# Optimization experiments

Measured on AMD Instinct MI355X. Metric: run time of the kernel, lower is better.

Reference implementation:

```python
import jax, jax.numpy as jnp
import numpy as np

B, L, H, E, MODES = 32, 2048, 8, 64, 64
SCALE = 1.0 / (512 * 512)  # 1/(in_channels*out_channels)


def setup_inputs() -> dict:
    key = jax.random.key(0)
    kq, kk, kv, kwr, kwi = jax.random.split(key, 5)
    # frequency mode selection: shuffled range(L//2), first MODES, sorted (get_frequency_modes)
    rng = np.random.default_rng(0)
    index = np.sort(rng.permutation(L // 2)[:MODES]).astype(np.int32)
    return {
        "q": jax.random.normal(kq, (B, L, H, E), dtype=jnp.float32),
        "k": jax.random.normal(kk, (B, L, H, E), dtype=jnp.float32),
        "v": jax.random.normal(kv, (B, L, H, E), dtype=jnp.float32),
        "w_real": SCALE * jax.random.uniform(kwr, (H, E, E, MODES), dtype=jnp.float32),
        "w_imag": SCALE * jax.random.uniform(kwi, (H, E, E, MODES), dtype=jnp.float32),
        "index": jnp.asarray(index),
    }


def reference(q, k, v, w_real, w_imag, index):
    # q: [B, L, H, E]; k, v unused by FourierBlock
    Bq, Lq, Hq, Eq = q.shape
    x = jnp.transpose(q, (0, 2, 3, 1))            # [B, H, E, L]
    x_ft = jnp.fft.rfft(x, axis=-1)               # [B, H, E, L//2+1] complex
    xs = jnp.take(x_ft, index, axis=-1)           # gather selected modes: [B, H, E, M]
    W = w_real + 1j * w_imag                      # [H, E, E, M] complex
    # vectorized per-mode complex einsum ('bhi,hio->bho' over all modes m)
    out = jnp.einsum('bhim,hiom->bhom', xs, W)    # [B, H, E, M]
    n_freq = Lq // 2 + 1
    # original writes mode wi into slot wi (0..M-1), rest stay zero
    out_ft = jnp.concatenate(
        [out, jnp.zeros((Bq, Hq, Eq, n_freq - out.shape[-1]), dtype=out.dtype)], axis=-1)
    return jnp.fft.irfft(out_ft, n=Lq, axis=-1)   # [B, H, E, L] real
```

## Files before the change

### kernel.cpp

```cpp
#include <hip/hip_runtime.h>
#include <math.h>

#define NB 32
#define NL 2048
#define NH 8
#define NE 64
#define NM 64
#define MRI 128
#define BK 128
#define NCH 16

typedef __attribute__((ext_vector_type(8))) __bf16 bf16x8;
typedef __attribute__((ext_vector_type(2))) __bf16 bf16x2;
typedef __attribute__((ext_vector_type(8))) unsigned short us8;
typedef __attribute__((ext_vector_type(4))) unsigned short us4;
typedef __attribute__((ext_vector_type(4))) float f32x4;
typedef __attribute__((ext_vector_type(16))) float f32x16;

__device__ __forceinline__ unsigned short f2bf(float x) {
  unsigned int u = __builtin_bit_cast(unsigned int, x);
  u = (u + 0x7fffu + ((u >> 16) & 1u)) >> 16;
  return (unsigned short)u;
}
__device__ __forceinline__ float bf2f(unsigned short u) {
  return __builtin_bit_cast(float, (unsigned int)u << 16);
}
__device__ __forceinline__ unsigned int pk2(float lo, float hi) {
  bf16x2 v;
  v[0] = (__bf16)lo;
  v[1] = (__bf16)hi;
  return __builtin_bit_cast(unsigned int, v);
}
__device__ __forceinline__ void gll16(const void* g, void* l) {
  __builtin_amdgcn_global_load_lds(
      (const __attribute__((address_space(1))) void*)g,
      (__attribute__((address_space(3))) void*)l, 16, 0, 0);
}
__device__ __forceinline__ void bar_lgkm() {
  asm volatile("s_waitcnt lgkmcnt(0)" ::: "memory");
  __builtin_amdgcn_s_barrier();
}

__global__ void tables_k(const int* __restrict__ idx,
                         const float* __restrict__ wr, const float* __restrict__ wi,
                         unsigned short* __restrict__ T, unsigned short* __restrict__ IT,
                         unsigned short* __restrict__ WBr, unsigned short* __restrict__ WBi) {
  int gid = blockIdx.x * blockDim.x + threadIdx.x;
  const float w0 = 6.283185307179586f / (float)NL;
  {
    int row = gid >> 11, l = gid & (NL - 1);
    int m = row & 63;
    int f = idx[m];
    float s, c;
    sincosf((float)((f * l) & (NL - 1)) * w0, &s, &c);
    T[gid] = f2bf(row < 64 ? c : -s);
  }
  {
    int lp = gid >> 7, k = gid & 127;
    int m = k & 63;
    float s, c;
    sincosf((float)((m * lp) & (NL - 1)) * w0, &s, &c);
    float v = (k < 64) ? ((m == 0 ? 1.0f : 2.0f) / (float)NL) * c
                       : (m == 0 ? 0.0f : (-2.0f / (float)NL) * s);
    IT[gid] = f2bf(v);
  }
  {
    const float2* wr2 = (const float2*)wr;
    const float2* wi2 = (const float2*)wi;
    unsigned int* obr = (unsigned int*)WBr;
    unsigned int* obi = (unsigned int*)WBi;
#pragma unroll
    for (int r = 0; r < 4; ++r) {
      int j = r * 262144 + gid;
      float2 a = wr2[j];
      float2 b2 = wi2[j];
      obr[j] = pk2(a.x, a.y);
      obi[j] = pk2(b2.x, b2.y);
    }
  }
}

__global__ __launch_bounds__(1024) void fused_k(const float* __restrict__ q,
                                                const unsigned short* __restrict__ T,
                                                const unsigned short* __restrict__ IT,
                                                const unsigned short* __restrict__ WBr,
                                                const unsigned short* __restrict__ WBi,
                                                float* __restrict__ out) {
  __shared__ __align__(16) char smem[99328];
  int t = threadIdx.x, lane = t & 63, wid = t >> 6;
  int h = blockIdx.x & 7, b = blockIdx.x >> 3;

  {
    char* Ab = smem;
    char* B0 = smem + 65536;
    char* B1 = smem + 65536 + 16896;
    const float* qb = q + ((size_t)b * NL * NH + h) * NE;
    int mh = wid >> 2, ehh = wid & 3;
    int eq = t & 15, lq = t >> 4;
    f32x4 acc[2] = {};
    f32x4 qA[2], qB[2];

    auto qload = [&](int c, f32x4* qr) {
#pragma unroll
      for (int p = 0; p < 2; ++p)
        qr[p] = *(const f32x4*)(qb + (size_t)(c * BK + lq * 2 + p) * (NH * NE) + eq * 4);
    };
    auto writesB = [&](const f32x4* qr, char* bb) {
#pragma unroll
      for (int j = 0; j < 4; ++j) {
        int e = eq * 4 + j;
        *(unsigned int*)(bb + e * 264 + lq * 4) = pk2(qr[0][j], qr[1][j]);
      }
    };
    auto stageA = [&](int bufi, int c) {
#pragma unroll
      for (int n = 0; n < 2; ++n) {
        int lin = n * 16384 + t * 16;
        int row = lin >> 8;
        int colb = (lin & 255) ^ ((row & 7) << 4);
        gll16((const char*)T + (size_t)row * (NL * 2) + (size_t)c * 256 + colb,
              Ab + bufi * 32768 + lin);
      }
    };
    auto compute = [&](const char* ab, const char* bb) {
#pragma unroll
      for (int ks2 = 0; ks2 < 4; ++ks2) {
        int e = ehh * 16 + (lane & 15);
        int boff = e * 264 + ks2 * 64 + (lane >> 4) * 16;
        uint2 blo = *(const uint2*)(bb + boff);
        uint2 bhi = *(const uint2*)(bb + boff + 8);
        bf16x8 bfr = __builtin_bit_cast(bf16x8, make_uint4(blo.x, blo.y, bhi.x, bhi.y));
#pragma unroll
        for (int fm = 0; fm < 2; ++fm) {
          int row = mh * 32 + fm * 16 + (lane & 15);
          int aoff = (row * 256 + ks2 * 64 + (lane >> 4) * 16) ^ ((row & 7) << 4);
          bf16x8 afr = __builtin_bit_cast(bf16x8, *(const us8*)(ab + aoff));
          acc[fm] = __builtin_amdgcn_mfma_f32_16x16x32_bf16(afr, bfr, acc[fm], 0, 0, 0);
        }
      }
    };

    qload(0, qA);
    qload(1, qB);
    stageA(0, 0);
    writesB(qA, B0);
    asm volatile("s_waitcnt vmcnt(0)" ::: "memory");
    __builtin_amdgcn_sched_barrier(0);
    bar_lgkm();
    for (int c = 0; c < 14; c += 2) {
      stageA(1, c + 1);
      qload(c + 2, qA);
      compute(Ab, B0);
      asm volatile("s_waitcnt vmcnt(2)" ::: "memory");
      __builtin_amdgcn_sched_barrier(0);
      __builtin_amdgcn_s_barrier();
      writesB(qB, B1);
      bar_lgkm();

      stageA(0, c + 2);
      qload(c + 3, qB);
      compute(Ab + 32768, B1);
      asm volatile("s_waitcnt vmcnt(2)" ::: "memory");
      __builtin_amdgcn_sched_barrier(0);
      __builtin_amdgcn_s_barrier();
      writesB(qA, B0);
      bar_lgkm();
    }
    stageA(1, 15);
    compute(Ab, B0);
    asm volatile("s_waitcnt vmcnt(0)" ::: "memory");
    __builtin_amdgcn_sched_barrier(0);
    __builtin_amdgcn_s_barrier();
    writesB(qB, B1);
    bar_lgkm();
    compute(Ab + 32768, B1);
    __syncthreads();
#pragma unroll
    for (int fm = 0; fm < 2; ++fm)
#pragma unroll
      for (int r4 = 0; r4 < 4; ++r4) {
        int row = mh * 32 + fm * 16 + (lane >> 4) * 4 + r4;
        int col = ehh * 16 + (lane & 15);
        int off = (row * 272 + col * 4) ^ (((row >> 3) & 7) << 4);
        *(float*)(smem + off) = acc[fm][r4];
      }
  }
  __syncthreads();

  {
    char* OtB = smem + 34816;
    int o = t >> 4, mq = t & 15;
    const unsigned short* wbr = WBr + (size_t)h * 262144 + o * 64 + mq * 4;
    const unsigned short* wbi = WBi + (size_t)h * 262144 + o * 64 + mq * 4;
    float orr[4] = {}, oii[4] = {};
    for (int ib = 0; ib < 16; ++ib) {
      f32x4 xr4[4], xi4[4];
#pragma unroll
      for (int mi = 0; mi < 4; ++mi) {
        int m = mq * 4 + mi;
        xr4[mi] = *(const f32x4*)(smem + ((m * 272 + ib * 16) ^ (((m >> 3) & 7) << 4)));
        xi4[mi] = *(const f32x4*)(smem + (((64 + m) * 272 + ib * 16) ^ (((m >> 3) & 7) << 4)));
      }
      us4 wr4[4], wi4[4];
#pragma unroll
      for (int ii = 0; ii < 4; ++ii) {
        int i = ib * 4 + ii;
        wr4[ii] = *(const us4*)(wbr + (size_t)i * 4096);
        wi4[ii] = *(const us4*)(wbi + (size_t)i * 4096);
      }
#pragma unroll
      for (int ii = 0; ii < 4; ++ii)
#pragma unroll
        for (int mi = 0; mi < 4; ++mi) {
          float wrv = bf2f(wr4[ii][mi]);
          float wiv = bf2f(wi4[ii][mi]);
          orr[mi] += xr4[mi][ii] * wrv - xi4[mi][ii] * wiv;
          oii[mi] += xr4[mi][ii] * wiv + xi4[mi][ii] * wrv;
        }
    }
    uint2 vr = make_uint2(pk2(orr[0], orr[1]), pk2(orr[2], orr[3]));
    uint2 vi = make_uint2(pk2(oii[0], oii[1]), pk2(oii[2], oii[3]));
    *(uint2*)(OtB + ((o * 256 + mq * 8) ^ ((o & 7) << 4))) = vr;
    *(uint2*)(OtB + ((o * 256 + 128 + mq * 8) ^ ((o & 7) << 4))) = vi;
  }
  __syncthreads();

  {
    const char* OtB = smem + 34816;
    bf16x8 af[2][8];
#pragma unroll
    for (int rg2 = 0; rg2 < 2; ++rg2)
#pragma unroll
      for (int ks = 0; ks < 8; ++ks) {
        int row = rg2 * 32 + (lane & 31);
        int off = (row * 256 + ks * 32 + (lane >> 5) * 16) ^ ((row & 7) << 4);
        af[rg2][ks] = __builtin_bit_cast(bf16x8, *(const us8*)(OtB + off));
      }
    float* ob = out + ((size_t)(b * 8 + h) * 64) * NL;
    int l0 = wid * 128;
    for (int ct = 0; ct < 4; ++ct) {
      int lr = l0 + ct * 32 + (lane & 31);
      f32x16 a2[2] = {};
#pragma unroll
      for (int ks = 0; ks < 8; ++ks) {
        bf16x8 bv = __builtin_bit_cast(
            bf16x8, *(const us8*)(IT + (size_t)lr * MRI + ks * 16 + (lane >> 5) * 8));
        a2[0] = __builtin_amdgcn_mfma_f32_32x32x16_bf16(af[0][ks], bv, a2[0], 0, 0, 0);
        a2[1] = __builtin_amdgcn_mfma_f32_32x32x16_bf16(af[1][ks], bv, a2[1], 0, 0, 0);
      }
#pragma unroll
      for (int rg2 = 0; rg2 < 2; ++rg2)
#pragma unroll
        for (int rg = 0; rg < 16; ++rg) {
          int row = rg2 * 32 + ((rg & 3) + 8 * (rg >> 2) + 4 * (lane >> 5));
          ob[(size_t)row * NL + lr] = a2[rg2][rg];
        }
    }
  }
}

extern "C" void kernel_launch(void* const* d_in, const int* in_sizes, int n_in,
                              void* d_out, int out_size, void* d_ws, size_t ws_size,
                              hipStream_t stream) {
  const float* q = (const float*)d_in[0];
  const float* wr = (const float*)d_in[3];
  const float* wi = (const float*)d_in[4];
  const int* idx = (const int*)d_in[5];
  float* out = (float*)d_out;
  char* ws = (char*)d_ws;

  constexpr size_t TBYTES = (size_t)MRI * NL * 2;
  constexpr size_t WBBYTES = (size_t)NH * NE * NE * NM * 2;
  constexpr size_t NEED = 2 * TBYTES + 2 * WBBYTES;
  if (ws_size < NEED) return;

  unsigned short* T = (unsigned short*)ws;
  unsigned short* IT = (unsigned short*)(ws + TBYTES);
  unsigned short* WBr = (unsigned short*)(ws + 2 * TBYTES);
  unsigned short* WBi = (unsigned short*)(ws + 2 * TBYTES + WBBYTES);

  hipLaunchKernelGGL(tables_k, dim3(1024), dim3(256), 0, stream, idx, wr, wi, T, IT, WBr, WBi);
  hipLaunchKernelGGL(fused_k, dim3(NB * NH), dim3(1024), 0, stream, q, T, IT, WBr, WBi, out);
}
```

Baseline: 87.17 us.

## Read fp32 weights directly, drop weight precast, restructure GEMM pipeline barriers

The weight conversion pass to bf16 in the table kernel is removed, and the mode-mixing stage now reads the fp32 weights directly. This eliminates an extra read and write of the weights, at the cost of loading twice as many bytes per block in the mixing stage. The forward-DFT GEMM loop is restructured with XOR-swizzled B tiles in place of padding, allowing single 16-byte LDS reads and one barrier per half-step instead of two. The inverse GEMM splits its accumulation into even and odd chains to increase MFMA independence.

```diff
diff --git a/kernel.cpp b/kernel.cpp
--- a/kernel.cpp
+++ b/kernel.cpp
@@ -13,7 +13,6 @@
 typedef __attribute__((ext_vector_type(8))) __bf16 bf16x8;
 typedef __attribute__((ext_vector_type(2))) __bf16 bf16x2;
 typedef __attribute__((ext_vector_type(8))) unsigned short us8;
-typedef __attribute__((ext_vector_type(4))) unsigned short us4;
 typedef __attribute__((ext_vector_type(4))) float f32x4;
 typedef __attribute__((ext_vector_type(16))) float f32x16;
 
@@ -21,9 +20,6 @@
   unsigned int u = __builtin_bit_cast(unsigned int, x);
   u = (u + 0x7fffu + ((u >> 16) & 1u)) >> 16;
   return (unsigned short)u;
-}
-__device__ __forceinline__ float bf2f(unsigned short u) {
-  return __builtin_bit_cast(float, (unsigned int)u << 16);
 }
 __device__ __forceinline__ unsigned int pk2(float lo, float hi) {
   bf16x2 v;
@@ -36,15 +32,9 @@
       (const __attribute__((address_space(1))) void*)g,
       (__attribute__((address_space(3))) void*)l, 16, 0, 0);
 }
-__device__ __forceinline__ void bar_lgkm() {
-  asm volatile("s_waitcnt lgkmcnt(0)" ::: "memory");
-  __builtin_amdgcn_s_barrier();
-}
 
 __global__ void tables_k(const int* __restrict__ idx,
-                         const float* __restrict__ wr, const float* __restrict__ wi,
-                         unsigned short* __restrict__ T, unsigned short* __restrict__ IT,
-                         unsigned short* __restrict__ WBr, unsigned short* __restrict__ WBi) {
+                         unsigned short* __restrict__ T, unsigned short* __restrict__ IT) {
   int gid = blockIdx.x * blockDim.x + threadIdx.x;
   const float w0 = 6.283185307179586f / (float)NL;
   {
@@ -64,36 +54,23 @@
                        : (m == 0 ? 0.0f : (-2.0f / (float)NL) * s);
     IT[gid] = f2bf(v);
   }
-  {
-    const float2* wr2 = (const float2*)wr;
-    const float2* wi2 = (const float2*)wi;
-    unsigned int* obr = (unsigned int*)WBr;
-    unsigned int* obi = (unsigned int*)WBi;
-#pragma unroll
-    for (int r = 0; r < 4; ++r) {
-      int j = r * 262144 + gid;
-      float2 a = wr2[j];
-      float2 b2 = wi2[j];
-      obr[j] = pk2(a.x, a.y);
-      obi[j] = pk2(b2.x, b2.y);
-    }
-  }
 }
 
 __global__ __launch_bounds__(1024) void fused_k(const float* __restrict__ q,
                                                 const unsigned short* __restrict__ T,
                                                 const unsigned short* __restrict__ IT,
-                                                const unsigned short* __restrict__ WBr,
-                                                const unsigned short* __restrict__ WBi,
+                                                const float* __restrict__ wr,
+                                                const float* __restrict__ wi,
                                                 float* __restrict__ out) {
-  __shared__ __align__(16) char smem[99328];
+  __shared__ __align__(16) char smem[98304];
   int t = threadIdx.x, lane = t & 63, wid = t >> 6;
   int h = blockIdx.x & 7, b = blockIdx.x >> 3;
 
   {
-    char* Ab = smem;
+    char* A0 = smem;
+    char* A1 = smem + 32768;
     char* B0 = smem + 65536;
-    char* B1 = smem + 65536 + 16896;
+    char* B1 = smem + 65536 + 16384;
     const float* qb = q + ((size_t)b * NL * NH + h) * NE;
     int mh = wid >> 2, ehh = wid & 3;
     int eq = t & 15, lq = t >> 4;
@@ -109,27 +86,26 @@
 #pragma unroll
       for (int j = 0; j < 4; ++j) {
         int e = eq * 4 + j;
-        *(unsigned int*)(bb + e * 264 + lq * 4) = pk2(qr[0][j], qr[1][j]);
-      }
-    };
-    auto stageA = [&](int bufi, int c) {
+        int sw = ((e ^ (e >> 2)) & 7) << 4;
+        *(unsigned int*)(bb + ((e * 256 + lq * 4) ^ sw)) = pk2(qr[0][j], qr[1][j]);
+      }
+    };
+    auto stageA = [&](char* ab, int c) {
 #pragma unroll
       for (int n = 0; n < 2; ++n) {
         int lin = n * 16384 + t * 16;
         int row = lin >> 8;
         int colb = (lin & 255) ^ ((row & 7) << 4);
-        gll16((const char*)T + (size_t)row * (NL * 2) + (size_t)c * 256 + colb,
-              Ab + bufi * 32768 + lin);
+        gll16((const char*)T + (size_t)row * (NL * 2) + (size_t)c * 256 + colb, ab + lin);
       }
     };
     auto compute = [&](const char* ab, const char* bb) {
 #pragma unroll
       for (int ks2 = 0; ks2 < 4; ++ks2) {
         int e = ehh * 16 + (lane & 15);
-        int boff = e * 264 + ks2 * 64 + (lane >> 4) * 16;
-        uint2 blo = *(const uint2*)(bb + boff);
-        uint2 bhi = *(const uint2*)(bb + boff + 8);
-        bf16x8 bfr = __builtin_bit_cast(bf16x8, make_uint4(blo.x, blo.y, bhi.x, bhi.y));
+        int bsw = ((e ^ (e >> 2)) & 7) << 4;
+        int boff = (e * 256 + ks2 * 64 + (lane >> 4) * 16) ^ bsw;
+        bf16x8 bfr = __builtin_bit_cast(bf16x8, *(const us8*)(bb + boff));
 #pragma unroll
         for (int fm = 0; fm < 2; ++fm) {
           int row = mh * 32 + fm * 16 + (lane & 15);
@@ -140,40 +116,40 @@
       }
     };
 
+    stageA(A0, 0);
     qload(0, qA);
     qload(1, qB);
-    stageA(0, 0);
     writesB(qA, B0);
+    asm volatile("s_waitcnt vmcnt(2)" ::: "memory");
+    __builtin_amdgcn_sched_barrier(0);
+    asm volatile("s_waitcnt lgkmcnt(0)" ::: "memory");
+    __builtin_amdgcn_s_barrier();
+    for (int c = 0; c < 14; c += 2) {
+      stageA(A1, c + 1);
+      qload(c + 2, qA);
+      compute(A0, B0);
+      writesB(qB, B1);
+      asm volatile("s_waitcnt vmcnt(2)" ::: "memory");
+      __builtin_amdgcn_sched_barrier(0);
+      asm volatile("s_waitcnt lgkmcnt(0)" ::: "memory");
+      __builtin_amdgcn_s_barrier();
+      stageA(A0, c + 2);
+      qload(c + 3, qB);
+      compute(A1, B1);
+      writesB(qA, B0);
+      asm volatile("s_waitcnt vmcnt(2)" ::: "memory");
+      __builtin_amdgcn_sched_barrier(0);
+      asm volatile("s_waitcnt lgkmcnt(0)" ::: "memory");
+      __builtin_amdgcn_s_barrier();
+    }
+    stageA(A1, 15);
+    compute(A0, B0);
+    writesB(qB, B1);
     asm volatile("s_waitcnt vmcnt(0)" ::: "memory");
     __builtin_amdgcn_sched_barrier(0);
-    bar_lgkm();
-    for (int c = 0; c < 14; c += 2) {
-      stageA(1, c + 1);
-      qload(c + 2, qA);
-      compute(Ab, B0);
-      asm volatile("s_waitcnt vmcnt(2)" ::: "memory");
-      __builtin_amdgcn_sched_barrier(0);
-      __builtin_amdgcn_s_barrier();
-      writesB(qB, B1);
-      bar_lgkm();
-
-      stageA(0, c + 2);
-      qload(c + 3, qB);
-      compute(Ab + 32768, B1);
-      asm volatile("s_waitcnt vmcnt(2)" ::: "memory");
-      __builtin_amdgcn_sched_barrier(0);
-      __builtin_amdgcn_s_barrier();
-      writesB(qA, B0);
-      bar_lgkm();
-    }
-    stageA(1, 15);
-    compute(Ab, B0);
-    asm volatile("s_waitcnt vmcnt(0)" ::: "memory");
-    __builtin_amdgcn_sched_barrier(0);
+    asm volatile("s_waitcnt lgkmcnt(0)" ::: "memory");
     __builtin_amdgcn_s_barrier();
-    writesB(qB, B1);
-    bar_lgkm();
-    compute(Ab + 32768, B1);
+    compute(A1, B1);
     __syncthreads();
 #pragma unroll
     for (int fm = 0; fm < 2; ++fm)
@@ -190,8 +166,8 @@
   {
     char* OtB = smem + 34816;
     int o = t >> 4, mq = t & 15;
-    const unsigned short* wbr = WBr + (size_t)h * 262144 + o * 64 + mq * 4;
-    const unsigned short* wbi = WBi + (size_t)h * 262144 + o * 64 + mq * 4;
+    const float* wrp = wr + (size_t)h * 262144 + (size_t)o * 64 + mq * 4;
+    const float* wip = wi + (size_t)h * 262144 + (size_t)o * 64 + mq * 4;
     float orr[4] = {}, oii[4] = {};
     for (int ib = 0; ib < 16; ++ib) {
       f32x4 xr4[4], xi4[4];
@@ -201,21 +177,19 @@
         xr4[mi] = *(const f32x4*)(smem + ((m * 272 + ib * 16) ^ (((m >> 3) & 7) << 4)));
         xi4[mi] = *(const f32x4*)(smem + (((64 + m) * 272 + ib * 16) ^ (((m >> 3) & 7) << 4)));
       }
-      us4 wr4[4], wi4[4];
+      f32x4 wr4[4], wi4[4];
 #pragma unroll
       for (int ii = 0; ii < 4; ++ii) {
         int i = ib * 4 + ii;
-        wr4[ii] = *(const us4*)(wbr + (size_t)i * 4096);
-        wi4[ii] = *(const us4*)(wbi + (size_t)i * 4096);
+        wr4[ii] = *(const f32x4*)(wrp + (size_t)i * 4096);
+        wi4[ii] = *(const f32x4*)(wip + (size_t)i * 4096);
       }
 #pragma unroll
       for (int ii = 0; ii < 4; ++ii)
 #pragma unroll
         for (int mi = 0; mi < 4; ++mi) {
-          float wrv = bf2f(wr4[ii][mi]);
-          float wiv = bf2f(wi4[ii][mi]);
-          orr[mi] += xr4[mi][ii] * wrv - xi4[mi][ii] * wiv;
-          oii[mi] += xr4[mi][ii] * wiv + xi4[mi][ii] * wrv;
+          orr[mi] += xr4[mi][ii] * wr4[ii][mi] - xi4[mi][ii] * wi4[ii][mi];
+          oii[mi] += xr4[mi][ii] * wi4[ii][mi] + xi4[mi][ii] * wr4[ii][mi];
         }
     }
     uint2 vr = make_uint2(pk2(orr[0], orr[1]), pk2(orr[2], orr[3]));
@@ -240,21 +214,27 @@
     int l0 = wid * 128;
     for (int ct = 0; ct < 4; ++ct) {
       int lr = l0 + ct * 32 + (lane & 31);
-      f32x16 a2[2] = {};
-#pragma unroll
-      for (int ks = 0; ks < 8; ++ks) {
-        bf16x8 bv = __builtin_bit_cast(
+      f32x16 aE[2] = {}, aO[2] = {};
+#pragma unroll
+      for (int ks = 0; ks < 8; ks += 2) {
+        bf16x8 bv0 = __builtin_bit_cast(
             bf16x8, *(const us8*)(IT + (size_t)lr * MRI + ks * 16 + (lane >> 5) * 8));
-        a2[0] = __builtin_amdgcn_mfma_f32_32x32x16_bf16(af[0][ks], bv, a2[0], 0, 0, 0);
-        a2[1] = __builtin_amdgcn_mfma_f32_32x32x16_bf16(af[1][ks], bv, a2[1], 0, 0, 0);
-      }
-#pragma unroll
-      for (int rg2 = 0; rg2 < 2; ++rg2)
+        bf16x8 bv1 = __builtin_bit_cast(
+            bf16x8, *(const us8*)(IT + (size_t)lr * MRI + (ks + 1) * 16 + (lane >> 5) * 8));
+        aE[0] = __builtin_amdgcn_mfma_f32_32x32x16_bf16(af[0][ks], bv0, aE[0], 0, 0, 0);
+        aE[1] = __builtin_amdgcn_mfma_f32_32x32x16_bf16(af[1][ks], bv0, aE[1], 0, 0, 0);
+        aO[0] = __builtin_amdgcn_mfma_f32_32x32x16_bf16(af[0][ks + 1], bv1, aO[0], 0, 0, 0);
+        aO[1] = __builtin_amdgcn_mfma_f32_32x32x16_bf16(af[1][ks + 1], bv1, aO[1], 0, 0, 0);
+      }
+#pragma unroll
+      for (int rg2 = 0; rg2 < 2; ++rg2) {
+        f32x16 a2 = aE[rg2] + aO[rg2];
 #pragma unroll
         for (int rg = 0; rg < 16; ++rg) {
           int row = rg2 * 32 + ((rg & 3) + 8 * (rg >> 2) + 4 * (lane >> 5));
-          ob[(size_t)row * NL + lr] = a2[rg2][rg];
+          ob[(size_t)row * NL + lr] = a2[rg];
         }
+      }
     }
   }
 }
@@ -270,15 +250,12 @@
   char* ws = (char*)d_ws;
 
   constexpr size_t TBYTES = (size_t)MRI * NL * 2;
-  constexpr size_t WBBYTES = (size_t)NH * NE * NE * NM * 2;
-  constexpr size_t NEED = 2 * TBYTES + 2 * WBBYTES;
+  constexpr size_t NEED = 2 * TBYTES;
   if (ws_size < NEED) return;
 
   unsigned short* T = (unsigned short*)ws;
   unsigned short* IT = (unsigned short*)(ws + TBYTES);
-  unsigned short* WBr = (unsigned short*)(ws + 2 * TBYTES);
-  unsigned short* WBi = (unsigned short*)(ws + 2 * TBYTES + WBBYTES);
-
-  hipLaunchKernelGGL(tables_k, dim3(1024), dim3(256), 0, stream, idx, wr, wi, T, IT, WBr, WBi);
-  hipLaunchKernelGGL(fused_k, dim3(NB * NH), dim3(1024), 0, stream, q, T, IT, WBr, WBi, out);
-}
+
+  hipLaunchKernelGGL(tables_k, dim3(1024), dim3(256), 0, stream, idx, T, IT);
+  hipLaunchKernelGGL(fused_k, dim3(NB * NH), dim3(1024), 0, stream, q, T, IT, wr, wi, out);
+}
```

After: 102.6 us. +17.7%, slower.

## Switch forward DFT GEMM to 32x32x16 MFMA with split-K across wave halves

Applied to the files above, without the earlier changes.

The forward transform GEMM now uses 32x32x16 bf16 MFMA tiles instead of pairs of 16x16x32 tiles. The 16 waves are split into two K halves that each accumulate over half of every chunk, and the partial sums are then reduced through LDS scratch. The aim is fewer MFMA issues and fewer fragment loads per wave. In exchange it adds an extra LDS reduction pass and a barrier, and it raises register pressure from the 16-wide accumulator. The mode-mixing loop also gets an unroll-2 hint.

```diff
diff --git a/kernel.cpp b/kernel.cpp
--- a/kernel.cpp
+++ b/kernel.cpp
@@ -35,10 +35,6 @@
   __builtin_amdgcn_global_load_lds(
       (const __attribute__((address_space(1))) void*)g,
       (__attribute__((address_space(3))) void*)l, 16, 0, 0);
-}
-__device__ __forceinline__ void bar_lgkm() {
-  asm volatile("s_waitcnt lgkmcnt(0)" ::: "memory");
-  __builtin_amdgcn_s_barrier();
 }
 
 __global__ void tables_k(const int* __restrict__ idx,
@@ -95,9 +91,11 @@
     char* B0 = smem + 65536;
     char* B1 = smem + 65536 + 16896;
     const float* qb = q + ((size_t)b * NL * NH + h) * NE;
-    int mh = wid >> 2, ehh = wid & 3;
+    int tm = wid & 3;
+    int te = (wid >> 2) & 1;
+    int kh = wid >> 3;
     int eq = t & 15, lq = t >> 4;
-    f32x4 acc[2] = {};
+    f32x16 acc32 = {};
     f32x4 qA[2], qB[2];
 
     auto qload = [&](int c, f32x4* qr) {
@@ -124,19 +122,17 @@
     };
     auto compute = [&](const char* ab, const char* bb) {
 #pragma unroll
-      for (int ks2 = 0; ks2 < 4; ++ks2) {
-        int e = ehh * 16 + (lane & 15);
-        int boff = e * 264 + ks2 * 64 + (lane >> 4) * 16;
+      for (int ks = 0; ks < 4; ++ks) {
+        int k0 = (kh * 4 + ks) * 16;
+        int e = te * 32 + (lane & 31);
+        int boff = e * 264 + (k0 + (lane >> 5) * 8) * 2;
         uint2 blo = *(const uint2*)(bb + boff);
         uint2 bhi = *(const uint2*)(bb + boff + 8);
         bf16x8 bfr = __builtin_bit_cast(bf16x8, make_uint4(blo.x, blo.y, bhi.x, bhi.y));
-#pragma unroll
-        for (int fm = 0; fm < 2; ++fm) {
-          int row = mh * 32 + fm * 16 + (lane & 15);
-          int aoff = (row * 256 + ks2 * 64 + (lane >> 4) * 16) ^ ((row & 7) << 4);
-          bf16x8 afr = __builtin_bit_cast(bf16x8, *(const us8*)(ab + aoff));
-          acc[fm] = __builtin_amdgcn_mfma_f32_16x16x32_bf16(afr, bfr, acc[fm], 0, 0, 0);
-        }
+        int row = tm * 32 + (lane & 31);
+        int aoff = (row * 256 + (k0 + (lane >> 5) * 8) * 2) ^ ((row & 7) << 4);
+        bf16x8 afr = __builtin_bit_cast(bf16x8, *(const us8*)(ab + aoff));
+        acc32 = __builtin_amdgcn_mfma_f32_32x32x16_bf16(afr, bfr, acc32, 0, 0, 0);
       }
     };
 
@@ -146,7 +142,8 @@
     writesB(qA, B0);
     asm volatile("s_waitcnt vmcnt(0)" ::: "memory");
     __builtin_amdgcn_sched_barrier(0);
-    bar_lgkm();
+    asm volatile("s_waitcnt lgkmcnt(0)" ::: "memory");
+    __builtin_amdgcn_s_barrier();
     for (int c = 0; c < 14; c += 2) {
       stageA(1, c + 1);
       qload(c + 2, qA);
@@ -155,7 +152,8 @@
       __builtin_amdgcn_sched_barrier(0);
       __builtin_amdgcn_s_barrier();
       writesB(qB, B1);
-      bar_lgkm();
+      asm volatile("s_waitcnt lgkmcnt(0)" ::: "memory");
+      __builtin_amdgcn_s_barrier();
 
       stageA(0, c + 2);
       qload(c + 3, qB);
@@ -164,7 +162,8 @@
       __builtin_amdgcn_sched_barrier(0);
       __builtin_amdgcn_s_barrier();
       writesB(qA, B0);
-      bar_lgkm();
+      asm volatile("s_waitcnt lgkmcnt(0)" ::: "memory");
+      __builtin_amdgcn_s_barrier();
     }
     stageA(1, 15);
     compute(Ab, B0);
@@ -172,18 +171,32 @@
     __builtin_amdgcn_sched_barrier(0);
     __builtin_amdgcn_s_barrier();
     writesB(qB, B1);
-    bar_lgkm();
+    asm volatile("s_waitcnt lgkmcnt(0)" ::: "memory");
+    __builtin_amdgcn_s_barrier();
     compute(Ab + 32768, B1);
     __syncthreads();
-#pragma unroll
-    for (int fm = 0; fm < 2; ++fm)
-#pragma unroll
-      for (int r4 = 0; r4 < 4; ++r4) {
-        int row = mh * 32 + fm * 16 + (lane >> 4) * 4 + r4;
-        int col = ehh * 16 + (lane & 15);
-        int off = (row * 272 + col * 4) ^ (((row >> 3) & 7) << 4);
-        *(float*)(smem + off) = acc[fm][r4];
-      }
+
+    float* scr = (float*)(smem + 65536);
+    int tile = wid & 7;
+    if (kh == 1) {
+#pragma unroll
+      for (int r = 0; r < 16; ++r) {
+        int row = (r & 3) + 8 * (r >> 2) + 4 * (lane >> 5);
+        scr[tile * 1024 + row * 32 + (lane & 31)] = acc32[r];
+      }
+    }
+    __syncthreads();
+    if (kh == 0) {
+#pragma unroll
+      for (int r = 0; r < 16; ++r) {
+        int row = (r & 3) + 8 * (r >> 2) + 4 * (lane >> 5);
+        float v = acc32[r] + scr[tile * 1024 + row * 32 + (lane & 31)];
+        int grow = tm * 32 + row;
+        int gcol = te * 32 + (lane & 31);
+        int off = (grow * 272 + gcol * 4) ^ (((grow >> 3) & 7) << 4);
+        *(float*)(smem + off) = v;
+      }
+    }
   }
   __syncthreads();
 
@@ -193,6 +206,7 @@
     const unsigned short* wbr = WBr + (size_t)h * 262144 + o * 64 + mq * 4;
     const unsigned short* wbi = WBi + (size_t)h * 262144 + o * 64 + mq * 4;
     float orr[4] = {}, oii[4] = {};
+#pragma unroll 2
     for (int ib = 0; ib < 16; ++ib) {
       f32x4 xr4[4], xi4[4];
 #pragma unroll
```

New measurement: 85.36 us. -2.1%, faster.
